# Performance work log

Hardware: AMD Instinct MI355X
Metric: run time of the kernel (lower is better)

The kernel has to match this reference:

```python
import jax, jax.numpy as jnp
import numpy as np

# dims: R ranks, B batch, HQ q-heads, HKV kv-heads-per-rank, G = HQ//HKV group size,
# D head dim, S kv splits (hardcoded 32 in module), L max kv len per rank, P pages per rank
R, B, HQ, HKV, D, S, L, P = 4, 16, 32, 2, 128, 32, 2048, 32768
G = HQ // HKV  # kv_group_num = num_q_heads // num_kv_heads_per_rank
NEG = -jnp.inf


def setup_inputs() -> dict:
    key = jax.random.key(0)
    k1, k2, k3, k4, k5 = jax.random.split(key, 5)
    q = jax.random.normal(k1, (B, HQ, D), jnp.float32)
    k_cache = jax.random.normal(k2, (R, P, HKV, D), jnp.float32)
    v_cache = jax.random.normal(k3, (R, P, HKV, D), jnp.float32)
    block_table = jax.random.randint(k4, (R, B, L), 0, P, jnp.int32)
    # per-rank kv lengths; min 64 to keep all math well-defined
    kv_lens_per_rank = jax.random.randint(k5, (R, B), 64, L + 1, jnp.int32)
    return dict(q=q, k_cache=k_cache, v_cache=v_cache,
                block_table=block_table, kv_lens_per_rank=kv_lens_per_rank)


def _attend(q, k_cache, v_cache, block_table, kv_lens):
    scale = D ** -0.5
    # page_size == 1: block_table entries are token slots in the per-rank cache.
    ridx = jnp.arange(R)[:, None, None]
    k = k_cache[ridx, block_table]  # [R,B,L,HKV,D]
    v = v_cache[ridx, block_table]  # [R,B,L,HKV,D]

    # GQA: q head h uses local kv head h // G on each rank
    qg = q.reshape(B, HKV, G, D)
    scores = jnp.einsum('bkgd,rblkd->rbkgl', qg, k) * scale  # [R,B,HKV,G,L]

    n = jnp.arange(L)
    valid = n[None, None, :] < kv_lens[..., None]            # [R,B,L]
    scores = jnp.where(valid[:, :, None, None, :], scores, NEG)

    # stage 1: split-KV. split s covers [s*per, (s+1)*per) with per = ceil(len/S)
    per = -(-kv_lens // S)                                   # [R,B]
    sid = n[None, None, :] // per[..., None]                 # [R,B,L]

    lse_s = []
    for s in range(S):  # fixed small loop over NUM_KV_SPLITS
        m = jnp.where((sid == s)[:, :, None, None, :], scores, NEG)
        lse_s.append(jax.scipy.special.logsumexp(m, axis=-1))  # [R,B,HKV,G]
    lse_s = jnp.stack(lse_s)  # [S,R,B,HKV,G]; empty splits -> -inf (kernel skips them)

    # stage 2: local combine over splits. NOTE (faithful to kernel): local_out stores
    # the UNNORMALIZED accumulator sum_s exp(lse_s - m_r) * o_s together with
    # lse_r = m_r + log(sum_s exp(lse_s - m_r)), where m_r = max_s lse_s.
    m_r = jnp.max(lse_s, axis=0)                              # [R,B,HKV,G]
    lse_r = m_r + jnp.log(jnp.sum(jnp.exp(lse_s - m_r), axis=0))
    # sum_s exp(lse_s - m_r) * (softmax_s @ v_s) == sum_n exp(score_n - m_r) * v_n
    p = jnp.exp(scores - m_r[..., None])                      # masked entries -> 0
    acc_r = jnp.einsum('rbkgl,rblkd->rbkgd', p, v)            # [R,B,HKV,G,D]

    acc = acc_r.reshape(R, B, HQ, D)
    lse = lse_r.reshape(R, B, HQ)

    # stage 3: global lse-weighted combine across ranks (online softmax == this)
    M = jnp.max(lse, axis=0)                                  # [B,HQ]
    w = jnp.exp(lse - M)                                      # [R,B,HQ]
    out = jnp.sum(w[..., None] * acc, axis=0) / jnp.sum(w, axis=0)[..., None]
    return out  # [B,HQ,D]


def reference(q, k_cache, v_cache, block_table, kv_lens_per_rank):
    return _attend(q, k_cache, v_cache, block_table, kv_lens_per_rank)
```

## Files before the change

kernel.cpp:

```cpp
#include <hip/hip_runtime.h>
#include <math.h>

#define R_ 4
#define B_ 16
#define HQ_ 32
#define HKV_ 2
#define G_ 16
#define D_ 128
#define S_ 32
#define L_ 2048
#define P_ 32768
#define TS_ 64
#define KSTR 136
#define PSTR 18
#define NEGINF (-INFINITY)

typedef _Float16 h2 __attribute__((ext_vector_type(2)));
typedef _Float16 h4 __attribute__((ext_vector_type(4)));
typedef _Float16 h8 __attribute__((ext_vector_type(8)));

#if defined(__has_builtin)
#  if __has_builtin(__builtin_amdgcn_fdot2)
#    define FDOT2(a,b,c) __builtin_amdgcn_fdot2((a),(b),(c),false)
#  endif
#endif
#ifndef FDOT2
static __device__ __forceinline__ float fdot2_sw(h2 a, h2 b, float c) {
  return c + (float)a.x*(float)b.x + (float)a.y*(float)b.y;
}
#  define FDOT2(a,b,c) fdot2_sw((a),(b),(c))
#endif


__global__ __launch_bounds__(256, 6) void fd_stage1(
    const float* __restrict__ q, const float* __restrict__ kc,
    const float* __restrict__ vc, const int* __restrict__ bt,
    const int* __restrict__ lens,
    float* __restrict__ lse_split, float* __restrict__ chunk_m,
    _Float16* __restrict__ chunk_acc)
{
  const int t   = threadIdx.x;
  const int blk = blockIdx.x;
  const int s   = blk & 31;
  const int hkv = (blk >> 5) & 1;
  const int b   = (blk >> 6) & 15;
  const int r   = blk >> 10;

  const int len = lens[r*B_ + b];
  const int per = (len + 31) >> 5;
  const int n0  = s*per;
  const int tn  = min(per, len - n0);

  float* lse_out = lse_split + ((r*B_ + b)*HKV_ + hkv)*(S_*G_);
  const int cmbase = (((r*B_ + b)*HKV_ + hkv)*S_ + s)*G_;
  _Float16* ca = chunk_acc + (size_t)(((r*B_ + b)*HKV_ + hkv)*S_ + s)*(G_*D_);

  if (tn <= 0) {
    if (t < G_) { lse_out[s*G_ + t] = NEGINF; chunk_m[cmbase + t] = NEGINF; }
    h8 z = {(_Float16)0,(_Float16)0,(_Float16)0,(_Float16)0,
            (_Float16)0,(_Float16)0,(_Float16)0,(_Float16)0};
    *(h8*)&ca[t*8] = z;
    return;
  }

  __shared__ _Float16 q_s[G_][KSTR];
  __shared__ _Float16 k_s[TS_][KSTR];
  __shared__ float    p_s[TS_][PSTR];

  {
    const float* qb = q + (b*HQ_ + hkv*G_)*D_;
    int f4 = t;
    #pragma unroll
    for (int i = 0; i < 2; ++i, f4 += 256) {
      const int g = f4 >> 5, dd = (f4 & 31)*4;
      const float4 v = *(const float4*)&qb[g*D_ + dd];
      h4 hv; hv.x=(_Float16)v.x; hv.y=(_Float16)v.y; hv.z=(_Float16)v.z; hv.w=(_Float16)v.w;
      *(h4*)&q_s[g][dd] = hv;
    }
  }

  const int* btb   = bt + (r*B_ + b)*L_;
  const int kvbase = r*(P_*HKV_*D_) + hkv*D_;

  {
    const int lane = t & 31, rw = t >> 5;
    for (int row = rw; row < tn; row += 8) {
      const int pg = btb[n0 + row];
      const float4 v = *(const float4*)&kc[kvbase + pg*(HKV_*D_) + lane*4];
      h4 hv; hv.x=(_Float16)v.x; hv.y=(_Float16)v.y; hv.z=(_Float16)v.z; hv.w=(_Float16)v.w;
      *(h4*)&k_s[row][lane*4] = hv;
    }
  }
  __syncthreads();

  const int sg = t >> 4, nl = t & 15;
  const int KN = (tn + 15) >> 4;
  float s0 = 0.f, s1 = 0.f, s2 = 0.f, s3 = 0.f;
  #pragma unroll 4
  for (int d8 = 0; d8 < 16; ++d8) {
    const h8 q8 = *(const h8*)&q_s[sg][d8*8];
    const h8 k0 = *(const h8*)&k_s[nl][d8*8];
    #pragma unroll
    for (int j = 0; j < 4; ++j) s0 = FDOT2(((const h2*)&q8)[j], ((const h2*)&k0)[j], s0);
    if (KN > 1) {
      const h8 k1 = *(const h8*)&k_s[nl + 16][d8*8];
      #pragma unroll
      for (int j = 0; j < 4; ++j) s1 = FDOT2(((const h2*)&q8)[j], ((const h2*)&k1)[j], s1);
    }
    if (KN > 2) {
      const h8 k2 = *(const h8*)&k_s[nl + 32][d8*8];
      #pragma unroll
      for (int j = 0; j < 4; ++j) s2 = FDOT2(((const h2*)&q8)[j], ((const h2*)&k2)[j], s2);
    }
    if (KN > 3) {
      const h8 k3 = *(const h8*)&k_s[nl + 48][d8*8];
      #pragma unroll
      for (int j = 0; j < 4; ++j) s3 = FDOT2(((const h2*)&q8)[j], ((const h2*)&k3)[j], s3);
    }
  }
  const float sc = 0.08838834764831845f;
  const float sv0 = (nl      < tn) ? s0*sc : NEGINF;
  const float sv1 = (nl + 16 < tn) ? s1*sc : NEGINF;
  const float sv2 = (nl + 32 < tn) ? s2*sc : NEGINF;
  const float sv3 = (nl + 48 < tn) ? s3*sc : NEGINF;

  float pm = fmaxf(fmaxf(sv0, sv1), fmaxf(sv2, sv3));
  #pragma unroll
  for (int off = 1; off < 16; off <<= 1) pm = fmaxf(pm, __shfl_xor(pm, off));
  float ps = __expf(sv0 - pm) + __expf(sv1 - pm) + __expf(sv2 - pm) + __expf(sv3 - pm);
  #pragma unroll
  for (int off = 1; off < 16; off <<= 1) ps += __shfl_xor(ps, off);

  if (nl == 0) {
    lse_out[s*G_ + sg] = pm + __logf(ps);
    chunk_m[cmbase + sg] = pm;
  }

  p_s[nl][sg] = __expf(sv0 - pm);
  if (KN > 1) p_s[nl + 16][sg] = __expf(sv1 - pm);
  if (KN > 2) p_s[nl + 32][sg] = __expf(sv2 - pm);
  if (KN > 3) p_s[nl + 48][sg] = __expf(sv3 - pm);
  __syncthreads();

  const int d4 = (t & 31)*4;
  const int g2 = (t >> 5)*2;
  float4 a0 = make_float4(0.f,0.f,0.f,0.f);
  float4 a1 = make_float4(0.f,0.f,0.f,0.f);
  #pragma unroll 4
  for (int n = 0; n < tn; ++n) {
    const int pg = btb[n0 + n];
    const float4 v4 = *(const float4*)&vc[kvbase + pg*(HKV_*D_) + d4];
    const float2 pp = *(const float2*)&p_s[n][g2];
    a0.x += pp.x*v4.x; a0.y += pp.x*v4.y; a0.z += pp.x*v4.z; a0.w += pp.x*v4.w;
    a1.x += pp.y*v4.x; a1.y += pp.y*v4.y; a1.z += pp.y*v4.z; a1.w += pp.y*v4.w;
  }

  h4 o0; o0.x=(_Float16)a0.x; o0.y=(_Float16)a0.y; o0.z=(_Float16)a0.z; o0.w=(_Float16)a0.w;
  h4 o1; o1.x=(_Float16)a1.x; o1.y=(_Float16)a1.y; o1.z=(_Float16)a1.z; o1.w=(_Float16)a1.w;
  *(h4*)&ca[g2*D_ + d4]       = o0;
  *(h4*)&ca[(g2 + 1)*D_ + d4] = o1;
}

__global__ __launch_bounds__(128) void fd_stage2(
    const float* __restrict__ lse_split, const float* __restrict__ chunk_m,
    const _Float16* __restrict__ chunk_acc, float* __restrict__ out)
{
  const int bh  = blockIdx.x;
  const int b   = bh >> 5, h = bh & 31;
  const int hkv = h >> 4, g = h & 15;
  const int d   = threadIdx.x;

  float m_r[R_], lse_r[R_];
  #pragma unroll
  for (int r = 0; r < R_; ++r) {
    const float* ls = lse_split + ((r*B_ + b)*HKV_ + hkv)*(S_*G_) + g;
    float m = NEGINF;
    #pragma unroll 8
    for (int s2 = 0; s2 < S_; ++s2) m = fmaxf(m, ls[s2*G_]);
    float sum = 0.f;
    #pragma unroll 8
    for (int s2 = 0; s2 < S_; ++s2) sum += __expf(ls[s2*G_] - m);
    m_r[r]   = m;
    lse_r[r] = m + __logf(sum);
  }
  const float M = fmaxf(fmaxf(lse_r[0], lse_r[1]), fmaxf(lse_r[2], lse_r[3]));
  float denom = 0.f, o = 0.f;
  #pragma unroll
  for (int r = 0; r < R_; ++r) {
    const float w = __expf(lse_r[r] - M);
    denom += w;
    const float* cm = chunk_m + (((r*B_ + b)*HKV_ + hkv)*S_)*G_ + g;
    const _Float16* ca = chunk_acc
        + (size_t)(((r*B_ + b)*HKV_ + hkv)*S_)*(G_*D_) + g*D_ + d;
    float a = 0.f;
    #pragma unroll 8
    for (int c = 0; c < S_; ++c)
      a += __expf(cm[c*G_] - m_r[r]) * (float)ca[(size_t)c*(G_*D_)];
    o += w * a;
  }
  out[(size_t)bh*D_ + d] = o / denom;
}

extern "C" void kernel_launch(void* const* d_in, const int* in_sizes, int n_in,
                              void* d_out, int out_size, void* d_ws, size_t ws_size,
                              hipStream_t stream) {
  const float* q   = (const float*)d_in[0];
  const float* kc  = (const float*)d_in[1];
  const float* vc  = (const float*)d_in[2];
  const int*   bt  = (const int*)d_in[3];
  const int*   len = (const int*)d_in[4];
  float* out = (float*)d_out;
  float* ws  = (float*)d_ws;

  const size_t lse_f = (size_t)R_*B_*HKV_*S_*G_;
  float*    lse_split = ws;
  float*    chunk_m   = ws + lse_f;
  _Float16* chunk_acc = (_Float16*)(ws + 2*lse_f);

  fd_stage1<<<dim3(R_*B_*HKV_*S_), dim3(256), 0, stream>>>(
      q, kc, vc, bt, len, lse_split, chunk_m, chunk_acc);
  fd_stage2<<<dim3(B_*HQ_), dim3(128), 0, stream>>>(
      lse_split, chunk_m, chunk_acc, out);
}
```

Before: 308.4 us.

## Compute QK scores with MFMA and cache page indices in shared memory

Replaces the per-thread fdot2 QK dot products with 16x16x32 f16 MFMA instructions, one wavefront per 16-token tile, and restructures the softmax max/sum reduction into a per-wave partial followed by a cross-wave combine through shared memory. The block-table page indices for the tile are also loaded once into shared memory and reused in the V accumulation loop, so the loop no longer rereads them from global memory. This adds extra barriers and a shared reduction buffer aliased onto p_s. The QK step is a small part of the block's work compared with the gathered K/V loads, so the overall effect may be limited.

```diff
diff --git a/kernel.cpp b/kernel.cpp
--- a/kernel.cpp
+++ b/kernel.cpp
@@ -15,21 +15,9 @@
 #define PSTR 18
 #define NEGINF (-INFINITY)
 
-typedef _Float16 h2 __attribute__((ext_vector_type(2)));
 typedef _Float16 h4 __attribute__((ext_vector_type(4)));
 typedef _Float16 h8 __attribute__((ext_vector_type(8)));
-
-#if defined(__has_builtin)
-#  if __has_builtin(__builtin_amdgcn_fdot2)
-#    define FDOT2(a,b,c) __builtin_amdgcn_fdot2((a),(b),(c),false)
-#  endif
-#endif
-#ifndef FDOT2
-static __device__ __forceinline__ float fdot2_sw(h2 a, h2 b, float c) {
-  return c + (float)a.x*(float)b.x + (float)a.y*(float)b.y;
-}
-#  define FDOT2(a,b,c) fdot2_sw((a),(b),(c))
-#endif
+typedef float    fx4 __attribute__((ext_vector_type(4)));
 
 
 __global__ __launch_bounds__(256, 6) void fd_stage1(
@@ -57,30 +45,33 @@
 
   if (tn <= 0) {
     if (t < G_) { lse_out[s*G_ + t] = NEGINF; chunk_m[cmbase + t] = NEGINF; }
-    h8 z = {(_Float16)0,(_Float16)0,(_Float16)0,(_Float16)0,
-            (_Float16)0,(_Float16)0,(_Float16)0,(_Float16)0};
+    h8 z = {};
     *(h8*)&ca[t*8] = z;
     return;
   }
 
   __shared__ _Float16 q_s[G_][KSTR];
   __shared__ _Float16 k_s[TS_][KSTR];
-  __shared__ float    p_s[TS_][PSTR];
+  __shared__ __align__(16) float p_s[TS_][PSTR];
+  __shared__ int pg_s[TS_];
+  float2* red = (float2*)&p_s[0][0];
+
+  const int* btb   = bt + (r*B_ + b)*L_;
+  const int kvbase = r*(P_*HKV_*D_) + hkv*D_;
+
+  if (t < TS_) pg_s[t] = btb[n0 + t];
 
   {
     const float* qb = q + (b*HQ_ + hkv*G_)*D_;
-    int f4 = t;
+    int fi = t;
     #pragma unroll
-    for (int i = 0; i < 2; ++i, f4 += 256) {
-      const int g = f4 >> 5, dd = (f4 & 31)*4;
+    for (int i = 0; i < 2; ++i, fi += 256) {
+      const int g = fi >> 5, dd = (fi & 31)*4;
       const float4 v = *(const float4*)&qb[g*D_ + dd];
       h4 hv; hv.x=(_Float16)v.x; hv.y=(_Float16)v.y; hv.z=(_Float16)v.z; hv.w=(_Float16)v.w;
       *(h4*)&q_s[g][dd] = hv;
     }
   }
-
-  const int* btb   = bt + (r*B_ + b)*L_;
-  const int kvbase = r*(P_*HKV_*D_) + hkv*D_;
 
   {
     const int lane = t & 31, rw = t >> 5;
@@ -93,53 +84,62 @@
   }
   __syncthreads();
 
-  const int sg = t >> 4, nl = t & 15;
-  const int KN = (tn + 15) >> 4;
-  float s0 = 0.f, s1 = 0.f, s2 = 0.f, s3 = 0.f;
-  #pragma unroll 4
-  for (int d8 = 0; d8 < 16; ++d8) {
-    const h8 q8 = *(const h8*)&q_s[sg][d8*8];
-    const h8 k0 = *(const h8*)&k_s[nl][d8*8];
+  const int w  = t >> 6;
+  const int l  = t & 63;
+  const int hh = l & 15;
+  const int tq = l >> 4;
+  const bool active = (16*w) < tn;
+
+  fx4 dacc = {0.f, 0.f, 0.f, 0.f};
+  if (active) {
     #pragma unroll
-    for (int j = 0; j < 4; ++j) s0 = FDOT2(((const h2*)&q8)[j], ((const h2*)&k0)[j], s0);
-    if (KN > 1) {
-      const h8 k1 = *(const h8*)&k_s[nl + 16][d8*8];
-      #pragma unroll
-      for (int j = 0; j < 4; ++j) s1 = FDOT2(((const h2*)&q8)[j], ((const h2*)&k1)[j], s1);
+    for (int c = 0; c < 4; ++c) {
+      const h8 af = *(const h8*)&k_s[16*w + hh][c*32 + 8*tq];
+      const h8 bf = *(const h8*)&q_s[hh][c*32 + 8*tq];
+      dacc = __builtin_amdgcn_mfma_f32_16x16x32_f16(af, bf, dacc, 0, 0, 0);
     }
-    if (KN > 2) {
-      const h8 k2 = *(const h8*)&k_s[nl + 32][d8*8];
-      #pragma unroll
-      for (int j = 0; j < 4; ++j) s2 = FDOT2(((const h2*)&q8)[j], ((const h2*)&k2)[j], s2);
-    }
-    if (KN > 3) {
-      const h8 k3 = *(const h8*)&k_s[nl + 48][d8*8];
-      #pragma unroll
-      for (int j = 0; j < 4; ++j) s3 = FDOT2(((const h2*)&q8)[j], ((const h2*)&k3)[j], s3);
-    }
-  }
+  }
+
   const float sc = 0.08838834764831845f;
-  const float sv0 = (nl      < tn) ? s0*sc : NEGINF;
-  const float sv1 = (nl + 16 < tn) ? s1*sc : NEGINF;
-  const float sv2 = (nl + 32 < tn) ? s2*sc : NEGINF;
-  const float sv3 = (nl + 48 < tn) ? s3*sc : NEGINF;
-
-  float pm = fmaxf(fmaxf(sv0, sv1), fmaxf(sv2, sv3));
-  #pragma unroll
-  for (int off = 1; off < 16; off <<= 1) pm = fmaxf(pm, __shfl_xor(pm, off));
-  float ps = __expf(sv0 - pm) + __expf(sv1 - pm) + __expf(sv2 - pm) + __expf(sv3 - pm);
-  #pragma unroll
-  for (int off = 1; off < 16; off <<= 1) ps += __shfl_xor(ps, off);
-
-  if (nl == 0) {
-    lse_out[s*G_ + sg] = pm + __logf(ps);
-    chunk_m[cmbase + sg] = pm;
-  }
-
-  p_s[nl][sg] = __expf(sv0 - pm);
-  if (KN > 1) p_s[nl + 16][sg] = __expf(sv1 - pm);
-  if (KN > 2) p_s[nl + 32][sg] = __expf(sv2 - pm);
-  if (KN > 3) p_s[nl + 48][sg] = __expf(sv3 - pm);
+  const int nb = 16*w + 4*tq;
+  const float sv0 = (nb + 0 < tn) ? dacc[0]*sc : NEGINF;
+  const float sv1 = (nb + 1 < tn) ? dacc[1]*sc : NEGINF;
+  const float sv2 = (nb + 2 < tn) ? dacc[2]*sc : NEGINF;
+  const float sv3 = (nb + 3 < tn) ? dacc[3]*sc : NEGINF;
+
+  float pmw = fmaxf(fmaxf(sv0, sv1), fmaxf(sv2, sv3));
+  pmw = fmaxf(pmw, __shfl_xor(pmw, 16));
+  pmw = fmaxf(pmw, __shfl_xor(pmw, 32));
+  const float pms = (pmw == NEGINF) ? 0.f : pmw;
+  const float e0 = __expf(sv0 - pms);
+  const float e1 = __expf(sv1 - pms);
+  const float e2 = __expf(sv2 - pms);
+  const float e3 = __expf(sv3 - pms);
+  float psw = e0 + e1 + e2 + e3;
+  psw += __shfl_xor(psw, 16);
+  psw += __shfl_xor(psw, 32);
+
+  if (l < 16) red[w*16 + l] = make_float2(pmw, psw);
+  __syncthreads();
+
+  const float2 rr0 = red[hh], rr1 = red[16 + hh], rr2 = red[32 + hh], rr3 = red[48 + hh];
+  const float pm = fmaxf(fmaxf(rr0.x, rr1.x), fmaxf(rr2.x, rr3.x));
+  const float ps = rr0.y*__expf(rr0.x - pm) + rr1.y*__expf(rr1.x - pm)
+                 + rr2.y*__expf(rr2.x - pm) + rr3.y*__expf(rr3.x - pm);
+
+  if (w == 0 && l < 16) {
+    lse_out[s*G_ + l]   = pm + __logf(ps);
+    chunk_m[cmbase + l] = pm;
+  }
+  __syncthreads();
+
+  if (active) {
+    const float cw = __expf(pmw - pm);
+    p_s[nb + 0][hh] = e0*cw;
+    p_s[nb + 1][hh] = e1*cw;
+    p_s[nb + 2][hh] = e2*cw;
+    p_s[nb + 3][hh] = e3*cw;
+  }
   __syncthreads();
 
   const int d4 = (t & 31)*4;
@@ -148,7 +148,7 @@
   float4 a1 = make_float4(0.f,0.f,0.f,0.f);
   #pragma unroll 4
   for (int n = 0; n < tn; ++n) {
-    const int pg = btb[n0 + n];
+    const int pg = pg_s[n];
     const float4 v4 = *(const float4*)&vc[kvbase + pg*(HKV_*D_) + d4];
     const float2 pp = *(const float2*)&p_s[n][g2];
     a0.x += pp.x*v4.x; a0.y += pp.x*v4.y; a0.z += pp.x*v4.z; a0.w += pp.x*v4.w;
```

New measurement: 305.7 us. No clear change (-0.9%).
